# Kernel optimization log

Hardware: AMD Instinct MI355X
Metric: run time of the kernel (lower is better)

## Reference

```python
import jax, jax.numpy as jnp
import numpy as np

EPS = 1e-6
NEG = -10000.0  # matches _merge_attn_masks neg_inf

def rms(x, w):
    return x * jax.lax.rsqrt(jnp.mean(x * x, axis=-1, keepdims=True) + EPS) * w

def setup_inputs() -> dict:
    key = jax.random.key(0)
    ks = jax.random.split(key, 16)
    B, Tq, Tk, D, H, G, dh, F, E = 4, 1024, 1024, 1024, 16, 4, 64, 4096, 8
    s = 1.0 / np.sqrt(D)
    sf = 1.0 / np.sqrt(F)
    return {
        "x": jax.random.normal(ks[0], (B, Tq, D), jnp.float32),
        "k_ctx": jax.random.normal(ks[1], (B, Tk, G, dh), jnp.float32),
        "v_ctx": jax.random.normal(ks[2], (B, Tk, G, dh), jnp.float32),
        "sa_norm_w": jnp.ones((D,), jnp.float32),
        "w_qkv": jax.random.normal(ks[3], (D, 3 * D), jnp.float32) * s,
        "sa_wout": jax.random.normal(ks[4], (D, D), jnp.float32) * s,
        "ca_norm_w": jnp.ones((D,), jnp.float32),
        "w_q": jax.random.normal(ks[5], (D, D), jnp.float32) * s,
        "ca_wout": jax.random.normal(ks[6], (D, D), jnp.float32) * s,
        "moe_norm_w": jnp.ones((D,), jnp.float32),
        "w_gate": jax.random.normal(ks[7], (D, E), jnp.float32) * s,
        "w1": jax.random.normal(ks[8], (E, D, F), jnp.float32) * s,
        "b1": jnp.zeros((E, F), jnp.float32),
        "w2": jax.random.normal(ks[9], (E, F, D), jnp.float32) * sf,
        "b2": jnp.zeros((E, D), jnp.float32),
    }

def _attn(q, k, v, mask=None):
    # q,k,v: [B,H,T,dh]
    dh = q.shape[-1]
    scores = jnp.einsum("bhqd,bhkd->bhqk", q, k) / jnp.sqrt(jnp.float32(dh))
    if mask is not None:
        scores = scores + mask
    p = jax.nn.softmax(scores, axis=-1)
    return jnp.einsum("bhqk,bhkd->bhqd", p, v)

def reference(x, k_ctx, v_ctx, sa_norm_w, w_qkv, sa_wout, ca_norm_w, w_q, ca_wout,
              moe_norm_w, w_gate, w1, b1, w2, b2):
    B, Tq, D = x.shape
    Tk, G, dh = k_ctx.shape[1], k_ctx.shape[2], k_ctx.shape[3]
    H = 16
    rep = H // G

    # ---- self-attention (causal, pre-norm RMS, residual) ----
    xn = rms(x, sa_norm_w)
    qkv = xn @ w_qkv  # [B,Tq,3D]
    q, k, v = jnp.split(qkv, 3, axis=-1)
    split = lambda t: t.reshape(B, Tq, H, dh).transpose(0, 2, 1, 3)
    i = jnp.arange(Tq)[:, None]
    j = jnp.arange(Tq)[None, :]
    causal = jnp.where(j <= i, 0.0, NEG).astype(jnp.float32)[None, None]
    y = _attn(split(q), split(k), split(v), causal)
    y = y.transpose(0, 2, 1, 3).reshape(B, Tq, D) @ sa_wout
    x = x + y

    # ---- cross-attention GQA ----
    qc = rms(x, ca_norm_w) @ w_q
    qc = qc.reshape(B, Tq, H, dh).transpose(0, 2, 1, 3)
    kk = jnp.repeat(k_ctx, rep, axis=2).transpose(0, 2, 1, 3)  # [B,H,Tk,dh]
    vv = jnp.repeat(v_ctx, rep, axis=2).transpose(0, 2, 1, 3)
    yc = _attn(qc, kk, vv)
    yc = yc.transpose(0, 2, 1, 3).reshape(B, Tq, D) @ ca_wout
    x = x + yc

    # ---- top-1 MoE FFN ----
    xm = rms(x, moe_norm_w)
    gate_scores = jax.nn.softmax(xm @ w_gate, axis=-1)  # [B,T,E]
    top1_idx = jnp.argmax(gate_scores, axis=-1)
    top1_score = jnp.max(gate_scores, axis=-1)
    E = w1.shape[0]
    out = jnp.zeros_like(xm)
    for e in range(E):  # small fixed expert count
        ye = jax.nn.silu(xm @ w1[e] + b1[e]) @ w2[e] + b2[e]
        out = jnp.where((top1_idx == e)[..., None], ye, out)
    out = out * top1_score[..., None]
    return x + out
```

## Files before the change

### kernel.cpp

```cpp
#include <hip/hip_runtime.h>
#include <hip/hip_bf16.h>
#include <stdint.h>

#define B_  4
#define T_  1024
#define D_  1024
#define H_  16
#define DH  64
#define F_  4096
#define E_  8
#define NT  (B_*T_)

typedef float f32x4 __attribute__((ext_vector_type(4)));
typedef short bf16x8 __attribute__((ext_vector_type(8)));
#define MFMA_BF16 __builtin_amdgcn_mfma_f32_16x16x32_bf16

union PK8 { uint32_t u[4]; bf16x8 v; };

#define GL16(gsrc, ldst)                                                      \
  __builtin_amdgcn_global_load_lds(                                           \
      (const __attribute__((address_space(1))) void*)(const void*)(gsrc),     \
      (__attribute__((address_space(3))) void*)(void*)(ldst), 16, 0, 0)

static __device__ __forceinline__ uint16_t f2bf(float f) {
  uint32_t u = __float_as_uint(f);
  u += 0x7FFFu + ((u >> 16) & 1u);
  return (uint16_t)(u >> 16);
}
static __device__ __forceinline__ void unpack8(const uint4 p0, const uint4 p1, bf16x8 &hi, bf16x8 &lo) {
  PK8 H, L;
  H.u[0] = __builtin_amdgcn_perm(p0.y, p0.x, 0x07060302u);
  L.u[0] = __builtin_amdgcn_perm(p0.y, p0.x, 0x05040100u);
  H.u[1] = __builtin_amdgcn_perm(p0.w, p0.z, 0x07060302u);
  L.u[1] = __builtin_amdgcn_perm(p0.w, p0.z, 0x05040100u);
  H.u[2] = __builtin_amdgcn_perm(p1.y, p1.x, 0x07060302u);
  L.u[2] = __builtin_amdgcn_perm(p1.y, p1.x, 0x05040100u);
  H.u[3] = __builtin_amdgcn_perm(p1.w, p1.z, 0x07060302u);
  L.u[3] = __builtin_amdgcn_perm(p1.w, p1.z, 0x05040100u);
  hi = H.v; lo = L.v;
}

__global__ __launch_bounds__(256) void k_pack_all(
    const float* __restrict__ wqkv, const float* __restrict__ saw,
    const float* __restrict__ wq,   const float* __restrict__ caw,
    uint16_t* __restrict__ qkvTh, uint16_t* __restrict__ qkvTl,
    uint16_t* __restrict__ sawTh, uint16_t* __restrict__ sawTl,
    uint16_t* __restrict__ wqTh,  uint16_t* __restrict__ wqTl,
    uint16_t* __restrict__ cawTh, uint16_t* __restrict__ cawTl) {
  __shared__ float t[32][33];
  int z = blockIdx.z;
  const float* in; uint16_t *oh, *ol; int N, nbase;
  if (z < 3)       { in = wqkv; oh = qkvTh; ol = qkvTl; N = 3072; nbase = z * 1024; }
  else if (z == 3) { in = saw;  oh = sawTh; ol = sawTl; N = 1024; nbase = 0; }
  else if (z == 4) { in = wq;   oh = wqTh;  ol = wqTl;  N = 1024; nbase = 0; }
  else             { in = caw;  oh = cawTh; ol = cawTl; N = 1024; nbase = 0; }
  int n0 = nbase + blockIdx.x * 32, k0 = blockIdx.y * 32;
  int tx = threadIdx.x & 31, ty = threadIdx.x >> 5;
#pragma unroll
  for (int i = 0; i < 32; i += 8) t[ty + i][tx] = in[(size_t)(k0 + ty + i) * N + n0 + tx];
  __syncthreads();
#pragma unroll
  for (int i = 0; i < 32; i += 8) {
    float v = t[tx][ty + i];
    uint16_t h = f2bf(v);
    uint16_t l = f2bf(v - __uint_as_float((uint32_t)h << 16));
    size_t o = (size_t)(n0 + ty + i) * 1024 + k0 + tx;
    oh[o] = h; ol[o] = l;
  }
}

__global__ __launch_bounds__(256) void k_bf_t2(const float* __restrict__ w1, const float* __restrict__ w2,
                                               uint16_t* __restrict__ w1t, uint16_t* __restrict__ w2t) {
  __shared__ float t[64][65];
  int z = blockIdx.z;
  int which = z >> 3, e = z & 7;
  const float* in = which ? w2 : w1;
  uint16_t* out = which ? w2t : w1t;
  int K = which ? F_ : D_, N = which ? D_ : F_;
  const size_t mo = (size_t)e * (size_t)D_ * F_;
  in += mo; out += mo;
  int tile = blockIdx.x;
  int n0, k0;
  if (which) { n0 = (tile & 15) * 64; k0 = (tile >> 4) * 64; }
  else       { n0 = (tile & 63) * 64; k0 = (tile >> 6) * 64; }
  int tr = threadIdx.x >> 4;
  int tc = (threadIdx.x & 15) * 4;
#pragma unroll
  for (int i = 0; i < 64; i += 16) {
    float4 v = *(const float4*)&in[(size_t)(k0 + tr + i) * N + n0 + tc];
    t[tr + i][tc] = v.x; t[tr + i][tc + 1] = v.y; t[tr + i][tc + 2] = v.z; t[tr + i][tc + 3] = v.w;
  }
  __syncthreads();
#pragma unroll
  for (int i = 0; i < 64; i += 16) {
    int n = tr + i;
    uint16_t b0 = f2bf(t[tc][n]), b1 = f2bf(t[tc + 1][n]);
    uint16_t b2 = f2bf(t[tc + 2][n]), b3 = f2bf(t[tc + 3][n]);
    uint2 wv;
    wv.x = ((uint32_t)b1 << 16) | b0;
    wv.y = ((uint32_t)b3 << 16) | b2;
    *(uint2*)&out[(size_t)(n0 + n) * K + k0 + tc] = wv;
  }
}

__global__ __launch_bounds__(256) void k_t16(const uint16_t* __restrict__ inh, const uint16_t* __restrict__ inl,
                                             uint16_t* __restrict__ outh, uint16_t* __restrict__ outl) {
  __shared__ uint16_t th[64][68], tl[64][68];
  int b = blockIdx.z, t0 = blockIdx.x * 64, c0 = blockIdx.y * 64;
  int tr = threadIdx.x >> 4;
  int tc = (threadIdx.x & 15) * 4;
#pragma unroll
  for (int i = 0; i < 64; i += 16) {
    size_t src = (size_t)(b * T_ + t0 + tr + i) * 3072 + 2048 + c0 + tc;
    *(uint2*)&th[tr + i][tc] = *(const uint2*)&inh[src];
    *(uint2*)&tl[tr + i][tc] = *(const uint2*)&inl[src];
  }
  __syncthreads();
#pragma unroll
  for (int i = 0; i < 64; i += 16) {
    int n = tr + i;
    size_t dst = (size_t)(b * 1024 + c0 + n) * T_ + t0 + tc;
    uint2 ph, pl;
    ph.x = ((uint32_t)th[tc + 1][n] << 16) | th[tc][n];
    ph.y = ((uint32_t)th[tc + 3][n] << 16) | th[tc + 2][n];
    pl.x = ((uint32_t)tl[tc + 1][n] << 16) | tl[tc][n];
    pl.y = ((uint32_t)tl[tc + 3][n] << 16) | tl[tc + 2][n];
    *(uint2*)&outh[dst] = ph;
    *(uint2*)&outl[dst] = pl;
  }
}

__global__ __launch_bounds__(256) void k_packf2(const float* __restrict__ in,
                                                uint16_t* __restrict__ oh, uint16_t* __restrict__ ol) {
  int i = (blockIdx.x * 256 + threadIdx.x) * 4;
  float4 v = *(const float4*)&in[i];
  uint16_t h0 = f2bf(v.x), h1 = f2bf(v.y), h2 = f2bf(v.z), h3 = f2bf(v.w);
  uint2 ph, pl;
  ph.x = ((uint32_t)h1 << 16) | h0;
  ph.y = ((uint32_t)h3 << 16) | h2;
  pl.x = ((uint32_t)f2bf(v.y - __uint_as_float((uint32_t)h1 << 16)) << 16) |
         f2bf(v.x - __uint_as_float((uint32_t)h0 << 16));
  pl.y = ((uint32_t)f2bf(v.w - __uint_as_float((uint32_t)h3 << 16)) << 16) |
         f2bf(v.z - __uint_as_float((uint32_t)h2 << 16));
  *(uint2*)&oh[i] = ph;
  *(uint2*)&ol[i] = pl;
}

__global__ __launch_bounds__(256) void k_tf32(const float* __restrict__ in,
                                              uint16_t* __restrict__ oh, uint16_t* __restrict__ ol) {
  __shared__ float t[32][33];
  int b = blockIdx.z, t0 = blockIdx.x * 32, c0 = blockIdx.y * 32;
  int tx = threadIdx.x & 31, ty = threadIdx.x >> 5;
#pragma unroll
  for (int i = 0; i < 32; i += 8)
    t[ty + i][tx] = in[(size_t)(b * T_ + t0 + ty + i) * 256 + c0 + tx];
  __syncthreads();
#pragma unroll
  for (int i = 0; i < 32; i += 8) {
    float v = t[tx][ty + i];
    uint16_t h = f2bf(v);
    size_t o = (size_t)(b * 256 + c0 + ty + i) * T_ + t0 + tx;
    oh[o] = h;
    ol[o] = f2bf(v - __uint_as_float((uint32_t)h << 16));
  }
}

__global__ __launch_bounds__(256) void k_rms(const float* __restrict__ x, const float* __restrict__ w,
                                             uint16_t* __restrict__ oh, uint16_t* __restrict__ ol,
                                             const float* __restrict__ wg, int* __restrict__ idxp,
                                             float* __restrict__ scb) {
  int row = blockIdx.x;
  const float* xr = x + (size_t)row * D_;
  int t = threadIdx.x;
  float4 xv = *(const float4*)&xr[t * 4];
  float s = xv.x * xv.x + xv.y * xv.y + xv.z * xv.z + xv.w * xv.w;
#pragma unroll
  for (int o = 32; o; o >>= 1) s += __shfl_xor(s, o, 64);
  __shared__ float ps[4];
  __shared__ float ga[4][8];
  if ((t & 63) == 0) ps[t >> 6] = s;
  __syncthreads();
  s = ps[0] + ps[1] + ps[2] + ps[3];
  float sc = 1.0f / sqrtf(s * (1.0f / (float)D_) + 1e-6f);
  float4 wv = *(const float4*)&w[t * 4];
  float o0 = xv.x * sc * wv.x, o1 = xv.y * sc * wv.y, o2 = xv.z * sc * wv.z, o3 = xv.w * sc * wv.w;
  uint16_t h0 = f2bf(o0), h1 = f2bf(o1), h2 = f2bf(o2), h3 = f2bf(o3);
  if (oh) {
    uint2 ph;
    ph.x = ((uint32_t)h1 << 16) | h0;
    ph.y = ((uint32_t)h3 << 16) | h2;
    *(uint2*)&oh[(size_t)row * D_ + t * 4] = ph;
  }
  if (ol) {
    uint16_t l0 = f2bf(o0 - __uint_as_float((uint32_t)h0 << 16));
    uint16_t l1 = f2bf(o1 - __uint_as_float((uint32_t)h1 << 16));
    uint16_t l2 = f2bf(o2 - __uint_as_float((uint32_t)h2 << 16));
    uint16_t l3 = f2bf(o3 - __uint_as_float((uint32_t)h3 << 16));
    uint2 pl;
    pl.x = ((uint32_t)l1 << 16) | l0;
    pl.y = ((uint32_t)l3 << 16) | l2;
    *(uint2*)&ol[(size_t)row * D_ + t * 4] = pl;
  }
  if (wg) {
    float a[8] = {};
    float ov[4] = {o0, o1, o2, o3};
#pragma unroll
    for (int j = 0; j < 4; j++) {
      const float* wr = &wg[(size_t)(t * 4 + j) * 8];
      float4 wa = *(const float4*)wr, wb = *(const float4*)(wr + 4);
      float v = ov[j];
      a[0] += v * wa.x; a[1] += v * wa.y; a[2] += v * wa.z; a[3] += v * wa.w;
      a[4] += v * wb.x; a[5] += v * wb.y; a[6] += v * wb.z; a[7] += v * wb.w;
    }
#pragma unroll
    for (int e = 0; e < 8; e++)
#pragma unroll
      for (int o = 32; o; o >>= 1) a[e] += __shfl_xor(a[e], o, 64);
    if ((t & 63) == 0)
#pragma unroll
      for (int e = 0; e < 8; e++) ga[t >> 6][e] = a[e];
    __syncthreads();
    if (t == 0) {
      float g[8];
#pragma unroll
      for (int e = 0; e < 8; e++) g[e] = ga[0][e] + ga[1][e] + ga[2][e] + ga[3][e];
      int bi = 0; float bv = g[0];
#pragma unroll
      for (int e = 1; e < 8; e++) if (g[e] > bv) { bv = g[e]; bi = e; }
      float se = 0.f;
#pragma unroll
      for (int e = 0; e < 8; e++) se += expf(g[e] - bv);
      idxp[row] = bi;
      scb[row] = 1.0f / se;
    }
  }
}

#define GBM 128
#define GBN 64
__global__ __launch_bounds__(256) void k_gemm_split(const uint16_t* __restrict__ Ahg, const uint16_t* __restrict__ Alg,
                                                    const uint16_t* __restrict__ Whg, const uint16_t* __restrict__ Wlg,
                                                    float* __restrict__ C, const float* __restrict__ res,
                                                    uint16_t* __restrict__ Cph, uint16_t* __restrict__ Cpl,
                                                    int scale_cols, int M, int N, int K) {
  __shared__ uint16_t Ah[2][GBM][32], Al[2][GBM][32];
  __shared__ uint16_t Wh[2][GBN][32], Wl[2][GBN][32];
  int m0 = blockIdx.y * GBM, n0 = blockIdx.x * GBN;
  int tid = threadIdx.x, wv = tid >> 6, ln = tid & 63, mi = ln & 15, b8 = ln >> 4;
  int lr = ln >> 2, lc = ln & 3;
  int cg = lc ^ (lr & 3);
  int rowA = wv * 32 + lr;
  int rowW = wv * 16 + lr;
  const uint16_t* pAh  = Ahg + (size_t)(m0 + rowA) * K + cg * 8;
  const uint16_t* pAl  = Alg + (size_t)(m0 + rowA) * K + cg * 8;
  const uint16_t* pAh2 = pAh + (size_t)16 * K;
  const uint16_t* pAl2 = pAl + (size_t)16 * K;
  const uint16_t* pWh  = Whg + (size_t)(n0 + rowW) * K + cg * 8;
  const uint16_t* pWl  = Wlg + (size_t)(n0 + rowW) * K + cg * 8;
  const int ch8 = (b8 ^ (mi & 3)) * 8;
  f32x4 acc[2][4] = {};

#define STAGE(bf) do {                                                         \
    GL16(pAh,  &Ah[bf][wv * 32][0]);                                           \
    GL16(pAh2, &Ah[bf][wv * 32 + 16][0]);                                      \
    GL16(pAl,  &Al[bf][wv * 32][0]);                                           \
    GL16(pAl2, &Al[bf][wv * 32 + 16][0]);                                      \
    GL16(pWh,  &Wh[bf][wv * 16][0]);                                           \
    GL16(pWl,  &Wl[bf][wv * 16][0]);                                           \
    pAh += 32; pAh2 += 32; pAl += 32; pAl2 += 32; pWh += 32; pWl += 32;        \
  } while (0)

  const int NK = K >> 5;
  STAGE(0);
  __syncthreads();
  int cur = 0;
  for (int t = 0; t < NK; ++t) {
    if (t + 1 < NK) STAGE(cur ^ 1);
    bf16x8 ah[2], al[2], bh[4], bl[4];
#pragma unroll
    for (int fm = 0; fm < 2; fm++) {
      ah[fm] = *(const bf16x8*)&Ah[cur][wv * 32 + fm * 16 + mi][ch8];
      al[fm] = *(const bf16x8*)&Al[cur][wv * 32 + fm * 16 + mi][ch8];
    }
#pragma unroll
    for (int fn = 0; fn < 4; fn++) {
      bh[fn] = *(const bf16x8*)&Wh[cur][fn * 16 + mi][ch8];
      bl[fn] = *(const bf16x8*)&Wl[cur][fn * 16 + mi][ch8];
    }
#pragma unroll
    for (int fm = 0; fm < 2; fm++)
#pragma unroll
      for (int fn = 0; fn < 4; fn++) {
        acc[fm][fn] = MFMA_BF16(al[fm], bh[fn], acc[fm][fn], 0, 0, 0);
        acc[fm][fn] = MFMA_BF16(ah[fm], bl[fn], acc[fm][fn], 0, 0, 0);
        acc[fm][fn] = MFMA_BF16(ah[fm], bh[fn], acc[fm][fn], 0, 0, 0);
      }
    __syncthreads();
    cur ^= 1;
  }
#undef STAGE
#pragma unroll
  for (int fm = 0; fm < 2; fm++)
#pragma unroll
    for (int fn = 0; fn < 4; fn++)
#pragma unroll
      for (int rr = 0; rr < 4; rr++) {
        int row = m0 + wv * 32 + fm * 16 + b8 * 4 + rr;
        int col = n0 + fn * 16 + mi;
        float v = acc[fm][fn][rr];
        size_t o = (size_t)row * N + col;
        if (Cph) {
          if (col < scale_cols) v *= 0.125f;
          uint16_t hv = f2bf(v);
          Cph[o] = hv;
          Cpl[o] = f2bf(v - __uint_as_float((uint32_t)hv << 16));
        } else {
          if (res) v += res[o];
          C[o] = v;
        }
      }
}

template <bool CAUSAL>
__global__ __launch_bounds__(256, 3) void k_fattn(
    const uint16_t* __restrict__ qhg, const uint16_t* __restrict__ qlg, int qs,
    const uint16_t* __restrict__ khg, const uint16_t* __restrict__ klg, int ks_, int khdiv,
    const uint16_t* __restrict__ vhg, const uint16_t* __restrict__ vlg, int nvrows,
    uint16_t* __restrict__ yhg, uint16_t* __restrict__ ylg) {
  __shared__ uint16_t Ksh[64][68], Ksl[64][68];
  __shared__ uint16_t Vsh[64][68], Vsl[64][68];
  __shared__ uint32_t Ps[4][32][36];
  const int h = blockIdx.y, b = blockIdx.z;
  const int qt = CAUSAL ? ((blockIdx.x + h + 2 * b) & 7) : blockIdx.x;
  const int tid = threadIdx.x, wv = tid >> 6, ln = tid & 63, mi = ln & 15, b8 = ln >> 4;
  const int koff = (h / khdiv) * 64;
  const uint16_t* kbh = khg + (size_t)b * T_ * ks_ + koff;
  const uint16_t* kbl = klg + (size_t)b * T_ * ks_ + koff;
  const uint16_t* vbh = vhg + ((size_t)b * nvrows + koff) * T_;
  const uint16_t* vbl = vlg + ((size_t)b * nvrows + koff) * T_;

  bf16x8 qh[2][2], ql[2][2];
#pragma unroll
  for (int u = 0; u < 2; u++)
#pragma unroll
    for (int k2 = 0; k2 < 2; k2++) {
      size_t o = (size_t)(b * T_ + qt * 128 + wv * 32 + u * 16 + mi) * qs + h * 64 + k2 * 32 + b8 * 8;
      qh[u][k2] = *(const bf16x8*)&qhg[o];
      ql[u][k2] = *(const bf16x8*)&qlg[o];
    }

  PK8 ONE_;
  ONE_.u[0] = 0x3F803F80u; ONE_.u[1] = 0x3F803F80u;
  ONE_.u[2] = 0x3F803F80u; ONE_.u[3] = 0x3F803F80u;
  const bf16x8 ones = ONE_.v;

  f32x4 lacc[2] = {};
  f32x4 o[2][4] = {};

  const int nkt = CAUSAL ? (2 * qt + 2) : (T_ / 64);
  for (int kt = 0; kt < nkt; kt++) {
    __syncthreads();
    {
      int rr = tid >> 2, cc = (tid & 3) * 16;
      size_t ko = (size_t)(kt * 64 + rr) * ks_ + cc;
      *(uint4*)&Ksh[rr][cc]     = *(const uint4*)&kbh[ko];
      *(uint4*)&Ksh[rr][cc + 8] = *(const uint4*)&kbh[ko + 8];
      *(uint4*)&Ksl[rr][cc]     = *(const uint4*)&kbl[ko];
      *(uint4*)&Ksl[rr][cc + 8] = *(const uint4*)&kbl[ko + 8];
      size_t vo = (size_t)rr * T_ + kt * 64 + cc;
      *(uint4*)&Vsh[rr][cc]     = *(const uint4*)&vbh[vo];
      *(uint4*)&Vsh[rr][cc + 8] = *(const uint4*)&vbh[vo + 8];
      *(uint4*)&Vsl[rr][cc]     = *(const uint4*)&vbl[vo];
      *(uint4*)&Vsl[rr][cc + 8] = *(const uint4*)&vbl[vo + 8];
    }
    __syncthreads();
#pragma unroll
    for (int s = 0; s < 2; s++) {
      bf16x8 kh[2][2], kl[2][2];
#pragma unroll
      for (int nf = 0; nf < 2; nf++)
#pragma unroll
        for (int k2 = 0; k2 < 2; k2++) {
          int rrow = s * 32 + nf * 16 + mi, ccol = k2 * 32 + b8 * 8;
          kh[nf][k2] = *(const bf16x8*)&Ksh[rrow][ccol];
          kl[nf][k2] = *(const bf16x8*)&Ksl[rrow][ccol];
        }
      f32x4 a[2][2] = {};
#pragma unroll
      for (int u = 0; u < 2; u++)
#pragma unroll
        for (int nf = 0; nf < 2; nf++)
#pragma unroll
          for (int k2 = 0; k2 < 2; k2++) {
            a[u][nf] = MFMA_BF16(ql[u][k2], kh[nf][k2], a[u][nf], 0, 0, 0);
            a[u][nf] = MFMA_BF16(qh[u][k2], kl[nf][k2], a[u][nf], 0, 0, 0);
            a[u][nf] = MFMA_BF16(qh[u][k2], kh[nf][k2], a[u][nf], 0, 0, 0);
          }
      if (CAUSAL && kt >= 2 * qt) {
        int kg = kt * 64 + s * 32 + mi;
#pragma unroll
        for (int u = 0; u < 2; u++) {
          int qg = qt * 128 + wv * 32 + u * 16 + b8 * 4;
#pragma unroll
          for (int r = 0; r < 4; r++) {
            if (kg > qg + r)      a[u][0][r] = -1e30f;
            if (kg + 16 > qg + r) a[u][1][r] = -1e30f;
          }
        }
      }
#pragma unroll
      for (int u = 0; u < 2; u++) {
#pragma unroll
        for (int r = 0; r < 4; r++) {
          a[u][0][r] = __expf(a[u][0][r]);
          a[u][1][r] = __expf(a[u][1][r]);
        }
#pragma unroll
        for (int r = 0; r < 4; r++) {
          uint32_t Hw, Lw;
          asm("v_cvt_pk_bf16_f32 %0, %1, %2" : "=v"(Hw) : "v"(a[u][0][r]), "v"(a[u][1][r]));
          float h0 = __uint_as_float(Hw << 16);
          float h1 = __uint_as_float(Hw & 0xffff0000u);
          float r0 = a[u][0][r] - h0, r1 = a[u][1][r] - h1;
          asm("v_cvt_pk_bf16_f32 %0, %1, %2" : "=v"(Lw) : "v"(r0), "v"(r1));
          Ps[wv][u * 16 + b8 * 4 + r][mi]      = __builtin_amdgcn_perm(Hw, Lw, 0x05040100u);
          Ps[wv][u * 16 + b8 * 4 + r][16 + mi] = __builtin_amdgcn_perm(Hw, Lw, 0x07060302u);
        }
      }
      bf16x8 ph[2], pl[2];
#pragma unroll
      for (int u = 0; u < 2; u++) {
        const uint32_t* p = &Ps[wv][u * 16 + mi][b8 * 8];
        unpack8(*(const uint4*)p, *(const uint4*)(p + 4), ph[u], pl[u]);
      }
#pragma unroll
      for (int u = 0; u < 2; u++) {
        lacc[u] = MFMA_BF16(pl[u], ones, lacc[u], 0, 0, 0);
        lacc[u] = MFMA_BF16(ph[u], ones, lacc[u], 0, 0, 0);
      }
#pragma unroll
      for (int f = 0; f < 4; f++) {
        int rrow = f * 16 + mi, ccol = s * 32 + b8 * 8;
        bf16x8 vh = *(const bf16x8*)&Vsh[rrow][ccol];
        bf16x8 vl = *(const bf16x8*)&Vsl[rrow][ccol];
#pragma unroll
        for (int u = 0; u < 2; u++) {
          o[u][f] = MFMA_BF16(pl[u], vh, o[u][f], 0, 0, 0);
          o[u][f] = MFMA_BF16(ph[u], vl, o[u][f], 0, 0, 0);
          o[u][f] = MFMA_BF16(ph[u], vh, o[u][f], 0, 0, 0);
        }
      }
    }
  }
#pragma unroll
  for (int u = 0; u < 2; u++)
#pragma unroll
    for (int r = 0; r < 4; r++) {
      float inv = 1.0f / lacc[u][r];
      int row = qt * 128 + wv * 32 + u * 16 + b8 * 4 + r;
#pragma unroll
      for (int f = 0; f < 4; f++) {
        size_t idx = (size_t)(b * T_ + row) * D_ + h * 64 + f * 16 + mi;
        float v = o[u][f][r] * inv;
        uint16_t hv = f2bf(v);
        yhg[idx] = hv;
        ylg[idx] = f2bf(v - __uint_as_float((uint32_t)hv << 16));
      }
    }
}

__global__ __launch_bounds__(256) void k_bucket(const int* __restrict__ idx, int* __restrict__ cnt,
                                                int* __restrict__ lists) {
  int tok = blockIdx.x * 256 + threadIdx.x;
  int e = idx[tok];
  int p = atomicAdd(&cnt[e], 1);
  lists[e * NT + p] = tok;
}

__global__ __launch_bounds__(256) void k_moe1(const uint16_t* __restrict__ xmbf, const uint16_t* __restrict__ w1t,
                                              const float* __restrict__ b1, const int* __restrict__ cnt,
                                              const int* __restrict__ lists, uint16_t* __restrict__ hbf) {
  int e = blockIdx.z;
  int c = cnt[e];
  int m0 = blockIdx.y * 64;
  if (m0 >= c) return;
  int n0 = blockIdx.x * 128;
  __shared__ uint16_t As[64][72];
  __shared__ uint16_t Ws[128][72];
  __shared__ int toks[64];
  int tid = threadIdx.x, wv = tid >> 6, ln = tid & 63, mi = ln & 15, b8 = ln >> 4;
  if (tid < 64) toks[tid] = (m0 + tid < c) ? lists[e * NT + m0 + tid] : -1;
  __syncthreads();
  int ra = tid >> 2, ca = (tid & 3) * 16;
  int rw = tid >> 1, cw = (tid & 1) * 32;
  int tk = toks[ra];
  const uint16_t* asrc = (tk >= 0) ? (xmbf + (size_t)tk * D_ + ca) : nullptr;
  const uint16_t* wsrc = w1t + (size_t)e * F_ * D_ + (size_t)(n0 + rw) * D_ + cw;
  f32x4 acc[4][2] = {};
  uint4 a0A = make_uint4(0,0,0,0), a1A = make_uint4(0,0,0,0), w0A, w1A, w2A, w3A;
  uint4 a0B = make_uint4(0,0,0,0), a1B = make_uint4(0,0,0,0), w0B, w1B, w2B, w3B;

#define M1LOAD(S, k0) do {                                                     \
    if (asrc) { a0##S = *(const uint4*)(asrc + (k0)); a1##S = *(const uint4*)(asrc + (k0) + 8); } \
    w0##S = *(const uint4*)(wsrc + (k0));      w1##S = *(const uint4*)(wsrc + (k0) + 8);  \
    w2##S = *(const uint4*)(wsrc + (k0) + 16); w3##S = *(const uint4*)(wsrc + (k0) + 24); \
  } while (0)
#define M1WRITE(S) do {                                                        \
    *(uint4*)&As[ra][ca] = a0##S;       *(uint4*)&As[ra][ca + 8] = a1##S;      \
    *(uint4*)&Ws[rw][cw] = w0##S;       *(uint4*)&Ws[rw][cw + 8] = w1##S;      \
    *(uint4*)&Ws[rw][cw + 16] = w2##S;  *(uint4*)&Ws[rw][cw + 24] = w3##S;     \
  } while (0)
#define M1COMPUTE() do {                                                       \
    _Pragma("unroll")                                                          \
    for (int ks = 0; ks < 2; ks++) {                                           \
      bf16x8 a[4], bb[2];                                                      \
      _Pragma("unroll")                                                        \
      for (int fm = 0; fm < 4; fm++)                                           \
        a[fm] = *(const bf16x8*)&As[fm * 16 + mi][ks * 32 + b8 * 8];           \
      _Pragma("unroll")                                                        \
      for (int nf = 0; nf < 2; nf++)                                           \
        bb[nf] = *(const bf16x8*)&Ws[wv * 32 + nf * 16 + mi][ks * 32 + b8 * 8];\
      _Pragma("unroll")                                                        \
      for (int fm = 0; fm < 4; fm++)                                           \
        _Pragma("unroll")                                                      \
        for (int nf = 0; nf < 2; nf++)                                         \
          acc[fm][nf] = MFMA_BF16(a[fm], bb[nf], acc[fm][nf], 0, 0, 0);        \
    }                                                                          \
  } while (0)

  M1LOAD(A, 0);
  M1WRITE(A);
  M1LOAD(B, 64);
  for (int k0 = 0; k0 < D_; k0 += 128) {
    __syncthreads();
    M1COMPUTE();
    __syncthreads();
    M1WRITE(B);
    if (k0 + 128 < D_) M1LOAD(A, k0 + 128);
    __syncthreads();
    M1COMPUTE();
    __syncthreads();
    if (k0 + 128 < D_) M1WRITE(A);
    if (k0 + 192 < D_) M1LOAD(B, k0 + 192);
  }
#undef M1LOAD
#undef M1WRITE
#undef M1COMPUTE
#pragma unroll
  for (int fm = 0; fm < 4; fm++)
#pragma unroll
    for (int nf = 0; nf < 2; nf++)
#pragma unroll
      for (int rr = 0; rr < 4; rr++) {
        int rt = fm * 16 + b8 * 4 + rr;
        if (m0 + rt < c) {
          int tok = toks[rt];
          int col = n0 + wv * 32 + nf * 16 + mi;
          float v = acc[fm][nf][rr] + b1[e * F_ + col];
          v = v / (1.0f + expf(-v));
          hbf[(size_t)tok * F_ + col] = f2bf(v);
        }
      }
}

__global__ __launch_bounds__(256) void k_moe2(const uint16_t* __restrict__ hbf, const uint16_t* __restrict__ w2t,
                                              const float* __restrict__ b2, const float* __restrict__ x2,
                                              const float* __restrict__ sc, const int* __restrict__ cnt,
                                              const int* __restrict__ lists, float* __restrict__ out) {
  int e = blockIdx.z;
  int c = cnt[e];
  int m0 = blockIdx.y * 64;
  if (m0 >= c) return;
  int n0 = blockIdx.x * 64;
  __shared__ uint16_t As[64][72];
  __shared__ uint16_t Ws[64][72];
  __shared__ int toks[64];
  int tid = threadIdx.x, wv = tid >> 6, ln = tid & 63, mi = ln & 15, b8 = ln >> 4;
  if (tid < 64) toks[tid] = (m0 + tid < c) ? lists[e * NT + m0 + tid] : -1;
  __syncthreads();
  int r = tid >> 2, c16 = (tid & 3) * 16;
  int tk = toks[r];
  const uint16_t* asrc = (tk >= 0) ? (hbf + (size_t)tk * F_ + c16) : nullptr;
  const uint16_t* wsrc = w2t + (size_t)e * D_ * F_ + (size_t)(n0 + r) * F_ + c16;
  f32x4 acc[4] = {};
  uint4 a0A = make_uint4(0,0,0,0), a1A = make_uint4(0,0,0,0), w0A, w1A;
  uint4 a0B = make_uint4(0,0,0,0), a1B = make_uint4(0,0,0,0), w0B, w1B;

#define M2LOAD(S, k0) do {                                                     \
    if (asrc) { a0##S = *(const uint4*)(asrc + (k0)); a1##S = *(const uint4*)(asrc + (k0) + 8); } \
    w0##S = *(const uint4*)(wsrc + (k0)); w1##S = *(const uint4*)(wsrc + (k0) + 8); \
  } while (0)
#define M2WRITE(S) do {                                                        \
    *(uint4*)&As[r][c16] = a0##S; *(uint4*)&As[r][c16 + 8] = a1##S;            \
    *(uint4*)&Ws[r][c16] = w0##S; *(uint4*)&Ws[r][c16 + 8] = w1##S;            \
  } while (0)
#define M2COMPUTE() do {                                                       \
    _Pragma("unroll")                                                          \
    for (int ks = 0; ks < 2; ks++) {                                           \
      bf16x8 a = *(const bf16x8*)&As[wv * 16 + mi][ks * 32 + b8 * 8];          \
      _Pragma("unroll")                                                        \
      for (int fn = 0; fn < 4; fn++) {                                         \
        bf16x8 bb = *(const bf16x8*)&Ws[fn * 16 + mi][ks * 32 + b8 * 8];       \
        acc[fn] = MFMA_BF16(a, bb, acc[fn], 0, 0, 0);                          \
      }                                                                        \
    }                                                                          \
  } while (0)

  M2LOAD(A, 0);
  M2WRITE(A);
  M2LOAD(B, 64);
  for (int k0 = 0; k0 < F_; k0 += 128) {
    __syncthreads();
    M2COMPUTE();
    __syncthreads();
    M2WRITE(B);
    if (k0 + 128 < F_) M2LOAD(A, k0 + 128);
    __syncthreads();
    M2COMPUTE();
    __syncthreads();
    if (k0 + 128 < F_) M2WRITE(A);
    if (k0 + 192 < F_) M2LOAD(B, k0 + 192);
  }
#undef M2LOAD
#undef M2WRITE
#undef M2COMPUTE
#pragma unroll
  for (int fn = 0; fn < 4; fn++)
#pragma unroll
    for (int rr = 0; rr < 4; rr++) {
      int rt = wv * 16 + b8 * 4 + rr;
      if (m0 + rt < c) {
        int tok = toks[rt];
        int col = n0 + fn * 16 + mi;
        float v = acc[fn][rr] + b2[e * D_ + col];
        out[(size_t)tok * D_ + col] = x2[(size_t)tok * D_ + col] + sc[tok] * v;
      }
    }
}

extern "C" void kernel_launch(void* const* d_in, const int* in_sizes, int n_in,
                              void* d_out, int out_size, void* d_ws, size_t ws_size,
                              hipStream_t stream) {
  const float* x       = (const float*)d_in[0];
  const float* k_ctx   = (const float*)d_in[1];
  const float* v_ctx   = (const float*)d_in[2];
  const float* sa_nw   = (const float*)d_in[3];
  const float* w_qkv   = (const float*)d_in[4];
  const float* sa_wout = (const float*)d_in[5];
  const float* ca_nw   = (const float*)d_in[6];
  const float* w_q     = (const float*)d_in[7];
  const float* ca_wout = (const float*)d_in[8];
  const float* moe_nw  = (const float*)d_in[9];
  const float* w_gate  = (const float*)d_in[10];
  const float* w1      = (const float*)d_in[11];
  const float* b1      = (const float*)d_in[12];
  const float* w2      = (const float*)d_in[13];
  const float* b2      = (const float*)d_in[14];
  float* out = (float*)d_out;
  (void)in_sizes; (void)n_in; (void)out_size; (void)ws_size;

  char* ws = (char*)d_ws;
  size_t off = 0;
  auto alloc = [&](size_t bytes) { char* p = ws + off; off += (bytes + 255) & ~(size_t)255; return p; };
  uint16_t* xnh   = (uint16_t*)alloc((size_t)NT * D_ * 2);
  uint16_t* xnl   = (uint16_t*)alloc((size_t)NT * D_ * 2);
  uint16_t* yh    = (uint16_t*)alloc((size_t)NT * D_ * 2);
  uint16_t* yl    = (uint16_t*)alloc((size_t)NT * D_ * 2);
  float*    x1    = (float*)alloc((size_t)NT * D_ * 4);
  uint16_t* qkvh  = (uint16_t*)alloc((size_t)NT * 3 * D_ * 2);
  uint16_t* qkvl  = (uint16_t*)alloc((size_t)NT * 3 * D_ * 2);
  float* x2 = (float*)qkvh;
  uint16_t* qch = qkvl;
  uint16_t* qcl = qkvl + (size_t)NT * D_;
  uint16_t* wqkvTh = (uint16_t*)alloc((size_t)D_ * 3 * D_ * 2);
  uint16_t* wqkvTl = (uint16_t*)alloc((size_t)D_ * 3 * D_ * 2);
  uint16_t* sawTh  = (uint16_t*)alloc((size_t)D_ * D_ * 2);
  uint16_t* sawTl  = (uint16_t*)alloc((size_t)D_ * D_ * 2);
  uint16_t* wqTh   = (uint16_t*)alloc((size_t)D_ * D_ * 2);
  uint16_t* wqTl   = (uint16_t*)alloc((size_t)D_ * D_ * 2);
  uint16_t* cawTh  = (uint16_t*)alloc((size_t)D_ * D_ * 2);
  uint16_t* cawTl  = (uint16_t*)alloc((size_t)D_ * D_ * 2);
  uint16_t* w1t   = (uint16_t*)alloc((size_t)E_ * D_ * F_ * 2);
  uint16_t* w2t   = (uint16_t*)alloc((size_t)E_ * D_ * F_ * 2);
  uint16_t* hbf   = (uint16_t*)alloc((size_t)NT * F_ * 2);
  uint16_t* vth   = (uint16_t*)hbf;
  uint16_t* vtl   = vth + (size_t)NT * D_;
  uint16_t* kch   = (uint16_t*)((char*)hbf + (size_t)16 * 1024 * 1024);
  uint16_t* kcl   = (uint16_t*)((char*)hbf + (size_t)18 * 1024 * 1024);
  uint16_t* vcth  = (uint16_t*)((char*)hbf + (size_t)20 * 1024 * 1024);
  uint16_t* vctl  = (uint16_t*)((char*)hbf + (size_t)22 * 1024 * 1024);
  uint16_t* xmbf  = (uint16_t*)alloc((size_t)NT * D_ * 2);
  int*   idx   = (int*)alloc(NT * 4);
  float* scb   = (float*)alloc(NT * 4);
  int*   cnt   = (int*)alloc(256);
  int*   lists = (int*)alloc((size_t)E_ * NT * 4);

  k_pack_all<<<dim3(32, 32, 6), 256, 0, stream>>>(w_qkv, sa_wout, w_q, ca_wout,
                                                  wqkvTh, wqkvTl, sawTh, sawTl,
                                                  wqTh, wqTl, cawTh, cawTl);
  k_bf_t2<<<dim3(1024, 1, 16), 256, 0, stream>>>(w1, w2, w1t, w2t);
  k_packf2<<<(B_ * T_ * 256) / 1024, 256, 0, stream>>>(k_ctx, kch, kcl);
  k_tf32<<<dim3(T_ / 32, 256 / 32, B_), 256, 0, stream>>>(v_ctx, vcth, vctl);

  k_rms<<<NT, 256, 0, stream>>>(x, sa_nw, xnh, xnl, nullptr, nullptr, nullptr);
  k_gemm_split<<<dim3(3 * D_ / GBN, NT / GBM), 256, 0, stream>>>(xnh, xnl, wqkvTh, wqkvTl, nullptr, nullptr, qkvh, qkvl, 1024, NT, 3 * D_, D_);
  k_t16<<<dim3(T_ / 64, D_ / 64, B_), 256, 0, stream>>>(qkvh, qkvl, vth, vtl);
  k_fattn<true><<<dim3(T_ / 128, H_, B_), 256, 0, stream>>>(qkvh, qkvl, 3072, qkvh + 1024, qkvl + 1024, 3072, 1, vth, vtl, 1024, yh, yl);
  k_gemm_split<<<dim3(D_ / GBN, NT / GBM), 256, 0, stream>>>(yh, yl, sawTh, sawTl, x1, x, nullptr, nullptr, 0, NT, D_, D_);

  k_rms<<<NT, 256, 0, stream>>>(x1, ca_nw, xnh, xnl, nullptr, nullptr, nullptr);
  k_gemm_split<<<dim3(D_ / GBN, NT / GBM), 256, 0, stream>>>(xnh, xnl, wqTh, wqTl, nullptr, nullptr, qch, qcl, 1024, NT, D_, D_);
  k_fattn<false><<<dim3(T_ / 128, H_, B_), 256, 0, stream>>>(qch, qcl, 1024, kch, kcl, 256, 4, vcth, vctl, 256, yh, yl);
  k_gemm_split<<<dim3(D_ / GBN, NT / GBM), 256, 0, stream>>>(yh, yl, cawTh, cawTl, x2, x1, nullptr, nullptr, 0, NT, D_, D_);

  k_rms<<<NT, 256, 0, stream>>>(x2, moe_nw, xmbf, nullptr, w_gate, idx, scb);
  hipMemsetAsync(cnt, 0, 32, stream);
  k_bucket<<<NT / 256, 256, 0, stream>>>(idx, cnt, lists);
  k_moe1<<<dim3(F_ / 128, NT / 64, E_), 256, 0, stream>>>(xmbf, w1t, b1, cnt, lists, hbf);
  k_moe2<<<dim3(D_ / 64, NT / 64, E_), 256, 0, stream>>>(hbf, w2t, b2, x2, scb, cnt, lists, out);
}
```

Before: 698.1 us.

## Replace LDS-direct double buffering with register-staged prefetch in split GEMM

The split-bf16 GEMM used global_load_lds to copy tiles straight into double-buffered shared memory. It now loads the next tiles into registers, keeps a single shared buffer, and writes the registers into shared memory after each compute step, with two register sets in flight. This halves LDS usage, which may allow higher occupancy, and hides global latency through register prefetch. The cost is more VGPRs, extra LDS write instructions, and four barriers per two k-steps instead of one per step.

Result: no change. 696.6 us (-0.2%).

```diff
diff --git a/kernel.cpp b/kernel.cpp
--- a/kernel.cpp
+++ b/kernel.cpp
@@ -16,11 +16,6 @@
 #define MFMA_BF16 __builtin_amdgcn_mfma_f32_16x16x32_bf16
 
 union PK8 { uint32_t u[4]; bf16x8 v; };
-
-#define GL16(gsrc, ldst)                                                      \
-  __builtin_amdgcn_global_load_lds(                                           \
-      (const __attribute__((address_space(1))) void*)(const void*)(gsrc),     \
-      (__attribute__((address_space(3))) void*)(void*)(ldst), 16, 0, 0)
 
 static __device__ __forceinline__ uint16_t f2bf(float f) {
   uint32_t u = __float_as_uint(f);
@@ -243,62 +238,77 @@
                                                     float* __restrict__ C, const float* __restrict__ res,
                                                     uint16_t* __restrict__ Cph, uint16_t* __restrict__ Cpl,
                                                     int scale_cols, int M, int N, int K) {
-  __shared__ uint16_t Ah[2][GBM][32], Al[2][GBM][32];
-  __shared__ uint16_t Wh[2][GBN][32], Wl[2][GBN][32];
+  __shared__ uint16_t Ah[GBM][32], Al[GBM][32];
+  __shared__ uint16_t Wh[GBN][32], Wl[GBN][32];
   int m0 = blockIdx.y * GBM, n0 = blockIdx.x * GBN;
   int tid = threadIdx.x, wv = tid >> 6, ln = tid & 63, mi = ln & 15, b8 = ln >> 4;
-  int lr = ln >> 2, lc = ln & 3;
-  int cg = lc ^ (lr & 3);
-  int rowA = wv * 32 + lr;
-  int rowW = wv * 16 + lr;
-  const uint16_t* pAh  = Ahg + (size_t)(m0 + rowA) * K + cg * 8;
-  const uint16_t* pAl  = Alg + (size_t)(m0 + rowA) * K + cg * 8;
-  const uint16_t* pAh2 = pAh + (size_t)16 * K;
-  const uint16_t* pAl2 = pAl + (size_t)16 * K;
-  const uint16_t* pWh  = Whg + (size_t)(n0 + rowW) * K + cg * 8;
-  const uint16_t* pWl  = Wlg + (size_t)(n0 + rowW) * K + cg * 8;
+  int ra = tid >> 1, ha = (tid & 1) * 2;
+  int rw = tid >> 2, hw = tid & 3;
+  const int sa0 = ((ha)     ^ (ra & 3)) * 8;
+  const int sa1 = ((ha + 1) ^ (ra & 3)) * 8;
+  const int sw  = (hw ^ (rw & 3)) * 8;
+  const uint16_t* baseAh = Ahg + (size_t)(m0 + ra) * K + ha * 8;
+  const uint16_t* baseAl = Alg + (size_t)(m0 + ra) * K + ha * 8;
+  const uint16_t* baseWh = Whg + (size_t)(n0 + rw) * K + hw * 8;
+  const uint16_t* baseWl = Wlg + (size_t)(n0 + rw) * K + hw * 8;
   const int ch8 = (b8 ^ (mi & 3)) * 8;
   f32x4 acc[2][4] = {};
-
-#define STAGE(bf) do {                                                         \
-    GL16(pAh,  &Ah[bf][wv * 32][0]);                                           \
-    GL16(pAh2, &Ah[bf][wv * 32 + 16][0]);                                      \
-    GL16(pAl,  &Al[bf][wv * 32][0]);                                           \
-    GL16(pAl2, &Al[bf][wv * 32 + 16][0]);                                      \
-    GL16(pWh,  &Wh[bf][wv * 16][0]);                                           \
-    GL16(pWl,  &Wl[bf][wv * 16][0]);                                           \
-    pAh += 32; pAh2 += 32; pAl += 32; pAl2 += 32; pWh += 32; pWl += 32;        \
-  } while (0)
-
-  const int NK = K >> 5;
-  STAGE(0);
-  __syncthreads();
-  int cur = 0;
-  for (int t = 0; t < NK; ++t) {
-    if (t + 1 < NK) STAGE(cur ^ 1);
-    bf16x8 ah[2], al[2], bh[4], bl[4];
-#pragma unroll
-    for (int fm = 0; fm < 2; fm++) {
-      ah[fm] = *(const bf16x8*)&Ah[cur][wv * 32 + fm * 16 + mi][ch8];
-      al[fm] = *(const bf16x8*)&Al[cur][wv * 32 + fm * 16 + mi][ch8];
-    }
-#pragma unroll
-    for (int fn = 0; fn < 4; fn++) {
-      bh[fn] = *(const bf16x8*)&Wh[cur][fn * 16 + mi][ch8];
-      bl[fn] = *(const bf16x8*)&Wl[cur][fn * 16 + mi][ch8];
-    }
-#pragma unroll
-    for (int fm = 0; fm < 2; fm++)
-#pragma unroll
-      for (int fn = 0; fn < 4; fn++) {
-        acc[fm][fn] = MFMA_BF16(al[fm], bh[fn], acc[fm][fn], 0, 0, 0);
-        acc[fm][fn] = MFMA_BF16(ah[fm], bl[fn], acc[fm][fn], 0, 0, 0);
-        acc[fm][fn] = MFMA_BF16(ah[fm], bh[fn], acc[fm][fn], 0, 0, 0);
-      }
-    __syncthreads();
-    cur ^= 1;
-  }
-#undef STAGE
+  uint4 ah0A, ah1A, al0A, al1A, whA, wlA;
+  uint4 ah0B, ah1B, al0B, al1B, whB, wlB;
+
+#define GLOAD(S, k0) do {                                                      \
+    ah0##S = *(const uint4*)(baseAh + (k0));                                   \
+    ah1##S = *(const uint4*)(baseAh + (k0) + 8);                               \
+    al0##S = *(const uint4*)(baseAl + (k0));                                   \
+    al1##S = *(const uint4*)(baseAl + (k0) + 8);                               \
+    wh##S  = *(const uint4*)(baseWh + (k0));                                   \
+    wl##S  = *(const uint4*)(baseWl + (k0));                                   \
+  } while (0)
+#define GWRITE(S) do {                                                         \
+    *(uint4*)&Ah[ra][sa0] = ah0##S; *(uint4*)&Ah[ra][sa1] = ah1##S;            \
+    *(uint4*)&Al[ra][sa0] = al0##S; *(uint4*)&Al[ra][sa1] = al1##S;            \
+    *(uint4*)&Wh[rw][sw]  = wh##S;  *(uint4*)&Wl[rw][sw]  = wl##S;             \
+  } while (0)
+#define GCOMPUTE() do {                                                        \
+    bf16x8 xah[2], xal[2], xbh[4], xbl[4];                                     \
+    _Pragma("unroll")                                                          \
+    for (int fm = 0; fm < 2; fm++) {                                           \
+      xah[fm] = *(const bf16x8*)&Ah[wv * 32 + fm * 16 + mi][ch8];              \
+      xal[fm] = *(const bf16x8*)&Al[wv * 32 + fm * 16 + mi][ch8];              \
+    }                                                                          \
+    _Pragma("unroll")                                                          \
+    for (int fn = 0; fn < 4; fn++) {                                           \
+      xbh[fn] = *(const bf16x8*)&Wh[fn * 16 + mi][ch8];                        \
+      xbl[fn] = *(const bf16x8*)&Wl[fn * 16 + mi][ch8];                        \
+    }                                                                          \
+    _Pragma("unroll")                                                          \
+    for (int fm = 0; fm < 2; fm++)                                             \
+      _Pragma("unroll")                                                        \
+      for (int fn = 0; fn < 4; fn++) {                                         \
+        acc[fm][fn] = MFMA_BF16(xal[fm], xbh[fn], acc[fm][fn], 0, 0, 0);       \
+        acc[fm][fn] = MFMA_BF16(xah[fm], xbl[fn], acc[fm][fn], 0, 0, 0);       \
+        acc[fm][fn] = MFMA_BF16(xah[fm], xbh[fn], acc[fm][fn], 0, 0, 0);       \
+      }                                                                        \
+  } while (0)
+
+  GLOAD(A, 0);
+  GWRITE(A);
+  GLOAD(B, 32);
+  for (int k0 = 0; k0 < K; k0 += 64) {
+    __syncthreads();
+    GCOMPUTE();
+    __syncthreads();
+    GWRITE(B);
+    if (k0 + 64 < K) GLOAD(A, k0 + 64);
+    __syncthreads();
+    GCOMPUTE();
+    __syncthreads();
+    if (k0 + 64 < K) GWRITE(A);
+    if (k0 + 96 < K) GLOAD(B, k0 + 96);
+  }
+#undef GLOAD
+#undef GWRITE
+#undef GCOMPUTE
 #pragma unroll
   for (int fm = 0; fm < 2; fm++)
 #pragma unroll
```
